# Kernel optimization log

Hardware: AMD Instinct MI355X
Metric: run time of the kernel (lower is better)

## Reference

```python
import jax, jax.numpy as jnp
import numpy as np

BN_EPS = 1e-3  # keras BatchNormalization default epsilon


def setup_inputs() -> dict:
    key = jax.random.key(0)
    ks = jax.random.split(key, 12)
    B, K, F = 32, 1024, 16
    H, C = 64, 4
    inp = {
        "x": jax.random.normal(ks[0], (B, K, F), dtype=jnp.float32),
        "coordinates": jax.random.normal(ks[1], (B, K, 3), dtype=jnp.float32),
        "precision_squared": jax.random.uniform(ks[2], (1,), dtype=jnp.float32),
        # dense kernels (no dense bias in the original; scalar per-block bias instead)
        "W0": 0.05 * jax.random.normal(ks[3], (2 * F, H), dtype=jnp.float32),
        "W1": 0.05 * jax.random.normal(ks[4], (4 * H, H), dtype=jnp.float32),
        "W2": 0.05 * jax.random.normal(ks[5], (4 * H, H), dtype=jnp.float32),
        "W3": 0.05 * jax.random.normal(ks[6], (4 * H, C), dtype=jnp.float32),
        "b0": 0.05 * jax.random.normal(ks[7], (1,), dtype=jnp.float32),
        "b1": 0.05 * jax.random.normal(ks[8], (1,), dtype=jnp.float32),
        "b2": 0.05 * jax.random.normal(ks[9], (1,), dtype=jnp.float32),
        "b3": 0.05 * jax.random.normal(ks[10], (1,), dtype=jnp.float32),
        # batchnorm affine params (inference mode, moving_mean=0, moving_var=1)
        "g0": jnp.ones((H,), jnp.float32), "be0": jnp.zeros((H,), jnp.float32),
        "g1": jnp.ones((H,), jnp.float32), "be1": jnp.zeros((H,), jnp.float32),
        "g2": jnp.ones((H,), jnp.float32), "be2": jnp.zeros((H,), jnp.float32),
    }
    return inp


def _adjacency(coordinates, precision_squared):
    # pairwise squared distances per sample: [B,K,K]
    norms = jnp.sum(coordinates * coordinates, axis=-1)  # [B,K]
    dist = norms[:, :, None] - 2.0 * jnp.einsum("bkd,bjd->bkj", coordinates, coordinates) + norms[:, None, :]
    A = jnp.exp(-dist * precision_squared[0])
    return jax.nn.softmax(A, axis=-1)  # per-sample axis=1 == last axis of [K,K]


def _block(x, A, W, b, gamma, beta, final):
    h = jnp.einsum("bij,bjf->bif", A, x)          # matmul(A, x)
    h = jnp.concatenate([h, x], axis=-1) @ W + b[0]
    if not final:
        # inference BN with moving_mean=0, moving_var=1
        h = h * (gamma / jnp.sqrt(1.0 + BN_EPS)) + beta
        h = jnp.concatenate([h, jax.nn.relu(h)], axis=-1)
    return h


def reference(x, coordinates, precision_squared, W0, W1, W2, W3,
              b0, b1, b2, b3, g0, be0, g1, be1, g2, be2):
    A = _adjacency(coordinates, precision_squared)
    h = _block(x, A, W0, b0, g0, be0, False)
    h = _block(h, A, W1, b1, g1, be1, False)
    h = _block(h, A, W2, b2, g2, be2, False)
    h = _block(h, A, W3, b3, None, None, True)   # final block: no BN, no activation
    h = jnp.mean(h, axis=1)                      # [B, num_classes]
    return jax.nn.softmax(h, axis=1)
```

## Files before the change

kernel.cpp:

```cpp
#include <hip/hip_runtime.h>
#include <math.h>

typedef __attribute__((ext_vector_type(8)))  __bf16   bf16x8;
typedef __attribute__((ext_vector_type(4)))  float    f32x4;
typedef __attribute__((ext_vector_type(16))) float    f32x16;
typedef __attribute__((ext_vector_type(4)))  unsigned u32x4;
typedef __attribute__((ext_vector_type(2)))  unsigned u32x2;

__device__ __forceinline__ unsigned short f2bf(float f) {
    unsigned u = __builtin_bit_cast(unsigned, f);
    u += 0x7fffu + ((u >> 16) & 1u);
    return (unsigned short)(u >> 16);
}
__device__ __forceinline__ float bf2f(unsigned short b) {
    unsigned u = ((unsigned)b) << 16;
    return __builtin_bit_cast(float, u);
}
__device__ __forceinline__ unsigned swz3(int key) { return (unsigned)((key ^ (key >> 3)) & 7); }
__device__ __forceinline__ bf16x8 ldfrag(const char* p) { return __builtin_bit_cast(bf16x8, *(const u32x4*)p); }

__global__ __launch_bounds__(256)
void prep(const float* __restrict__ W0, const float* __restrict__ W1,
          const float* __restrict__ W2, const float* __restrict__ W3,
          unsigned short* __restrict__ wpk)
{
    int id = blockIdx.x * 256 + threadIdx.x;
    if (id >= 51200) return;
    float v;
    if (id < 2048) {
        int j = id;
        int e = j & 7, lane = (j >> 3) & 63, nt = (j >> 9) & 3;
        int f = ((lane >> 5) << 3) + e + ((nt >= 2) ? 16 : 0);
        int h = ((nt & 1) << 5) + (lane & 31);
        v = W0[f * 64 + h];
    } else {
        int jid = id - 2048;
        int l = jid >> 14;
        int j = jid & 16383;
        int e = j & 7, lane = (j >> 3) & 63, nt = (j >> 9) & 3, kk = j >> 11;
        int f = kk * 16 + ((lane >> 5) << 3) + e + ((nt >= 2) ? 128 : 0);
        int h = ((nt & 1) << 5) + (lane & 31);
        const float* W = (l == 0) ? W1 : (l == 1) ? W2 : W3;
        int H = (l == 2) ? 4 : 64;
        v = (h < H) ? W[f * H + h] : 0.f;
    }
    wpk[id] = f2bf(v);
}

__global__ __launch_bounds__(256, 3)
void tgen(const float* __restrict__ coords, const float* __restrict__ psq,
          unsigned short* __restrict__ Tg, float* __restrict__ pcol)
{
    __shared__ float4 sc[1152];
    __shared__ char   tile[16 * 2048];
    const int t = threadIdx.x;
    const int b = blockIdx.y;
    const int i0 = blockIdx.x * 16;
    for (int k = t; k < 1024; k += 256) {
        const float* c = coords + ((size_t)b*1024 + k)*3;
        float cx = c[0], cy = c[1], cz = c[2];
        sc[k + (k >> 3)] = make_float4(cx, cy, cz, cx*cx + cy*cy + cz*cz);
    }
    __syncthreads();
    const float p = psq[0];
    const int r = t >> 4, jg = t & 15;
    const int kci = i0 + r;
    const float4 ci = sc[kci + (kci >> 3)];
    u32x4 raw[8];
    float rsum = 0.f;
#pragma unroll
    for (int pp = 0; pp < 8; ++pp) {
        const int base = pp*144 + jg*9;
        u32x4 v;
#pragma unroll
        for (int e = 0; e < 4; ++e) {
            float4 cj0 = sc[base + 2*e], cj1 = sc[base + 2*e + 1];
            float d0 = ci.w + cj0.w - 2.f*(ci.x*cj0.x + ci.y*cj0.y + ci.z*cj0.z);
            float d1 = ci.w + cj1.w - 2.f*(ci.x*cj1.x + ci.y*cj1.y + ci.z*cj1.z);
            unsigned short h0 = f2bf(__expf(__expf(-d0 * p)));
            unsigned short h1 = f2bf(__expf(__expf(-d1 * p)));
            rsum += bf2f(h0) + bf2f(h1);
            v[e] = (unsigned)h0 | ((unsigned)h1 << 16);
        }
        raw[pp] = v;
    }
    rsum += __shfl_xor(rsum, 1);
    rsum += __shfl_xor(rsum, 2);
    rsum += __shfl_xor(rsum, 4);
    rsum += __shfl_xor(rsum, 8);
    const float rinv = 1.f / rsum;
    char* trow = tile + r * 2048;
#pragma unroll
    for (int pp = 0; pp < 8; ++pp) {
        u32x4 u = raw[pp], v;
#pragma unroll
        for (int e = 0; e < 4; ++e) {
            unsigned uu = u[e];
            unsigned short nl = f2bf(bf2f((unsigned short)(uu & 0xffffu)) * rinv);
            unsigned short nh = f2bf(bf2f((unsigned short)(uu >> 16)) * rinv);
            v[e] = (unsigned)nl | ((unsigned)nh << 16);
        }
        *(u32x4*)(trow + (pp*128 + jg*8)*2) = v;
    }
    __syncthreads();
    {
        const int j0 = t * 4;
        f32x4 cs = {0.f, 0.f, 0.f, 0.f};
#pragma unroll
        for (int rr = 0; rr < 16; ++rr) {
            u32x2 u = *(const u32x2*)(tile + rr*2048 + j0*2);
            cs[0] += bf2f((unsigned short)(u[0] & 0xffffu));
            cs[1] += bf2f((unsigned short)(u[0] >> 16));
            cs[2] += bf2f((unsigned short)(u[1] & 0xffffu));
            cs[3] += bf2f((unsigned short)(u[1] >> 16));
        }
        *(f32x4*)(pcol + ((size_t)(b*64 + blockIdx.x))*1024 + j0) = cs;
    }
    {
        const u32x4* src = (const u32x4*)tile;
        u32x4* dst = (u32x4*)(Tg + ((size_t)(b*1024 + i0))*1024);
        for (int v = t; v < 2048; v += 256) dst[v] = src[v];
    }
}

__global__ __launch_bounds__(256, 2)
void proj0(const float* __restrict__ x32, const unsigned short* __restrict__ wpk,
           const float* __restrict__ bias, unsigned short* __restrict__ vuT)
{
    __shared__ char smem[2048 + 4096 + 16384];
    constexpr int XS = 0, WS = 2048, TBO = 6144;
    const int t = threadIdx.x;
    const int l = t & 63, w = t >> 6;
    const int b = blockIdx.y;
    const int i0g = blockIdx.x * 64;
    const int m31 = l & 31, kg = l >> 5;
    const int mi = w & 1, ntb = (w >> 1) * 2;
    const float bv = bias[0];

    {
        const int i = t >> 2, q = t & 3;
        const float* s = x32 + ((size_t)(b*1024 + i0g + i))*16 + q*4;
        unsigned short h0 = f2bf(s[0]), h1 = f2bf(s[1]), h2 = f2bf(s[2]), h3 = f2bf(s[3]);
        u32x2 v = {(unsigned)h0 | ((unsigned)h1 << 16), (unsigned)h2 | ((unsigned)h3 << 16)};
        *(u32x2*)(smem + XS + i*32 + ((q*8) ^ ((i & 1) << 4))) = v;
    }
    {
        u32x4* dstw = (u32x4*)(smem + WS);
        const u32x4* srcw = (const u32x4*)wpk;
        if (t < 256) dstw[t] = srcw[t];
    }
    __syncthreads();

    f32x16 acc0, acc1;
#pragma unroll
    for (int r = 0; r < 16; ++r) { acc0[r] = 0.f; acc1[r] = 0.f; }
    const int arow = mi*32 + m31;
    const char* ap = smem + XS + arow * 32;
    const unsigned swA = (unsigned)(arow & 1) << 4;
    {
        bf16x8 a  = ldfrag(ap + ((kg*16) ^ swA));
        bf16x8 b0 = ldfrag(smem + WS + (ntb    )*1024 + l*16);
        bf16x8 b1 = ldfrag(smem + WS + (ntb + 1)*1024 + l*16);
        acc0 = __builtin_amdgcn_mfma_f32_32x32x16_bf16(a, b0, acc0, 0, 0, 0);
        acc1 = __builtin_amdgcn_mfma_f32_32x32x16_bf16(a, b1, acc1, 0, 0, 0);
    }
    __syncthreads();
#pragma unroll
    for (int ntp = 0; ntp < 2; ++ntp) {
        const int nt = ntb + ntp;
        const int prow = nt*32 + m31;
        char* tb = smem + TBO + prow*128;
        const unsigned sw = (unsigned)(prow & 7) << 4;
        const float badd = (nt >= 2) ? bv : 0.f;
#pragma unroll
        for (int r = 0; r < 16; ++r) {
            const int i = mi*32 + (r & 3) + 8*(r >> 2) + 4*kg;
            float z = ((ntp == 0) ? acc0[r] : acc1[r]) + badd;
            *(unsigned short*)(tb + ((i*2) ^ sw)) = f2bf(z);
        }
    }
    __syncthreads();
    {
        const int hh = t >> 1, q = t & 1;
        const char* tb = smem + TBO + hh*128;
        const unsigned sw = (unsigned)(hh & 7) << 4;
        unsigned short* g = vuT + ((size_t)(b*128 + hh))*1024 + i0g + q*32;
#pragma unroll
        for (int gg = 0; gg < 4; ++gg) {
            u32x4 v = *(const u32x4*)(tb + ((q*64 + gg*16) ^ sw));
            *(u32x4*)(g + gg*8) = v;
        }
    }
}

__global__ __launch_bounds__(256, 2)
void fspmm(const unsigned short* __restrict__ vuT, const unsigned short* __restrict__ P,
           const float* __restrict__ gamma, const float* __restrict__ beta,
           const unsigned short* __restrict__ wpkN, const float* __restrict__ biasN,
           unsigned short* __restrict__ ovuT)
{
    __shared__ char smem[32768];
    const int t = threadIdx.x;
    const int l = t & 63, w = t >> 6;
    const int b = blockIdx.y;
    const int i0g = blockIdx.x * 64;
    const int m31 = l & 31, kg = l >> 5;
    const int wh = w >> 1, wi2 = w & 1;
    const float bvN = biasN[0];

    const int r4 = t >> 2, c4 = t & 3;
    const unsigned short* gp = P   + ((size_t)(b*1024 + i0g + r4))*1024 + c4*16;
    const unsigned short* gv = vuT + ((size_t)(b*128 + r4))*1024 + c4*16;
    u32x4 rp0 = *(const u32x4*)(gp), rp1 = *(const u32x4*)(gp + 8);
    u32x4 rv0 = *(const u32x4*)(gv), rv1 = *(const u32x4*)(gv + 8);
    const unsigned swr = swz3(r4) << 4;
    const int aRow = wh*32 + m31, bRow = wi2*32 + m31;
    const unsigned swA = swz3(aRow) << 4, swB = swz3(bRow) << 4;

    f32x16 acc;
#pragma unroll
    for (int r = 0; r < 16; ++r) acc[r] = 0.f;

    for (int jt = 0; jt < 16; ++jt) {
        const int p = jt & 1;
        {
            char* pt = smem + p*8192 + r4*128;
            *(u32x4*)(pt + ((c4*32     ) ^ swr)) = rp0;
            *(u32x4*)(pt + ((c4*32 + 16) ^ swr)) = rp1;
            char* vt = smem + 16384 + p*8192 + r4*128;
            *(u32x4*)(vt + ((c4*32     ) ^ swr)) = rv0;
            *(u32x4*)(vt + ((c4*32 + 16) ^ swr)) = rv1;
        }
        if (jt < 15) {
            rp0 = *(const u32x4*)(gp + (jt+1)*64);
            rp1 = *(const u32x4*)(gp + (jt+1)*64 + 8);
            rv0 = *(const u32x4*)(gv + (jt+1)*64);
            rv1 = *(const u32x4*)(gv + (jt+1)*64 + 8);
        }
        __syncthreads();
        const char* a_ = smem + 16384 + p*8192 + aRow*128;
        const char* b_ = smem + p*8192 + bRow*128;
#pragma unroll
        for (int kk = 0; kk < 4; ++kk) {
            const unsigned off = kk*32 + kg*16;
            bf16x8 af = ldfrag(a_ + (off ^ swA));
            bf16x8 bf = ldfrag(b_ + (off ^ swB));
            acc = __builtin_amdgcn_mfma_f32_32x32x16_bf16(af, bf, acc, 0, 0, 0);
        }
        __syncthreads();
    }

    {
        const unsigned short* gu = vuT + ((size_t)(b*128 + 64 + r4))*1024 + i0g + c4*16;
        u32x4 u0 = *(const u32x4*)(gu), u1 = *(const u32x4*)(gu + 8);
        *(u32x4*)(smem + r4*128 + c4*32)      = u0;
        *(u32x4*)(smem + r4*128 + c4*32 + 16) = u1;
    }
    __syncthreads();
    const float bns = rsqrtf(1.f + 1e-3f);
    const int ii = wi2*32 + m31;
    char* ZT = smem + 16384;
    const unsigned swzi = (unsigned)(ii & 7) << 4;
#pragma unroll
    for (int r = 0; r < 16; ++r) {
        const int h = wh*32 + (r & 3) + 8*(r >> 2) + 4*kg;
        float u = bf2f(*(const unsigned short*)(smem + h*128 + ii*2));
        float z = (acc[r] + u) * (gamma[h] * bns) + beta[h];
        *(unsigned short*)(ZT + ii*256 + (((unsigned)(h*2)) ^ swzi))        = f2bf(z);
        *(unsigned short*)(ZT + ii*256 + (((unsigned)((64 + h)*2)) ^ swzi)) = f2bf(fmaxf(z, 0.f));
    }
    __syncthreads();

    f32x16 vac, uac;
#pragma unroll
    for (int r = 0; r < 16; ++r) { vac[r] = 0.f; uac[r] = bvN; }
    const char* bx_base = ZT + ii*256;
#pragma unroll
    for (int kk = 0; kk < 8; ++kk) {
        bf16x8 awv = __builtin_bit_cast(bf16x8, *(const u32x4*)(wpkN + ((size_t)((kk*4 + wh    )*64 + l))*8));
        bf16x8 awu = __builtin_bit_cast(bf16x8, *(const u32x4*)(wpkN + ((size_t)((kk*4 + wh + 2)*64 + l))*8));
        bf16x8 bx  = ldfrag(bx_base + ((kk*32 + kg*16) ^ swzi));
        vac = __builtin_amdgcn_mfma_f32_32x32x16_bf16(awv, bx, vac, 0, 0, 0);
        uac = __builtin_amdgcn_mfma_f32_32x32x16_bf16(awu, bx, uac, 0, 0, 0);
    }
    __syncthreads();
    {
        char* TB = smem;
#pragma unroll
        for (int r = 0; r < 16; ++r) {
            const int hv = wh*32 + (r & 3) + 8*(r >> 2) + 4*kg;
            const unsigned sw = (unsigned)(hv & 7) << 4;
            *(unsigned short*)(TB + hv*128        + ((ii*2) ^ sw)) = f2bf(vac[r]);
            *(unsigned short*)(TB + (hv + 64)*128 + ((ii*2) ^ sw)) = f2bf(uac[r]);
        }
    }
    __syncthreads();
    {
        const int hh = t >> 1, q = t & 1;
        const char* tb = smem + hh*128;
        const unsigned sw = (unsigned)(hh & 7) << 4;
        unsigned short* g = ovuT + ((size_t)(b*128 + hh))*1024 + i0g + q*32;
#pragma unroll
        for (int gg = 0; gg < 4; ++gg) {
            u32x4 v = *(const u32x4*)(tb + ((q*64 + gg*16) ^ sw));
            *(u32x4*)(g + gg*8) = v;
        }
    }
}

__global__ __launch_bounds__(256)
void finalize(const float* __restrict__ pcol, const unsigned short* __restrict__ vuT3,
              float* __restrict__ out)
{
    __shared__ float red[2056];
    const int b = blockIdx.x, t = threadIdx.x;
    const int j0 = t * 4;
    f32x4 cs = {0.f, 0.f, 0.f, 0.f};
    for (int p = 0; p < 64; ++p)
        cs += *(const f32x4*)(pcol + ((size_t)(b*64 + p))*1024 + j0);
    float lv[4], lu[4];
#pragma unroll
    for (int h = 0; h < 4; ++h) {
        const unsigned short* vr = vuT3 + ((size_t)(b*128 + h))*1024 + j0;
        lv[h] = cs[0]*bf2f(vr[0]) + cs[1]*bf2f(vr[1]) + cs[2]*bf2f(vr[2]) + cs[3]*bf2f(vr[3]);
        const unsigned short* ur = vuT3 + ((size_t)(b*128 + 64 + h))*1024 + j0;
        lu[h] = bf2f(ur[0]) + bf2f(ur[1]) + bf2f(ur[2]) + bf2f(ur[3]);
    }
#pragma unroll
    for (int q = 0; q < 4; ++q) { red[t*8 + q] = lv[q]; red[t*8 + 4 + q] = lu[q]; }
    __syncthreads();
    if (t < 8) {
        float s = 0.f;
        for (int k = 0; k < 256; ++k) s += red[k*8 + t];
        red[2048 + t] = s;
    }
    __syncthreads();
    if (t == 0) {
        float v[4];
#pragma unroll
        for (int h = 0; h < 4; ++h) v[h] = (red[2048 + h] + red[2048 + 4 + h]) * (1.f / 1024.f);
        const float m = fmaxf(fmaxf(v[0], v[1]), fmaxf(v[2], v[3]));
        float e[4], se = 0.f;
#pragma unroll
        for (int h = 0; h < 4; ++h) { e[h] = __expf(v[h] - m); se += e[h]; }
        const float inv = 1.f / se;
#pragma unroll
        for (int h = 0; h < 4; ++h) out[b*4 + h] = e[h] * inv;
    }
}

extern "C" void kernel_launch(void* const* d_in, const int* in_sizes, int n_in,
                              void* d_out, int out_size, void* d_ws, size_t ws_size,
                              hipStream_t stream)
{
    const float* x   = (const float*)d_in[0];
    const float* co  = (const float*)d_in[1];
    const float* psq = (const float*)d_in[2];
    const float* W0  = (const float*)d_in[3];
    const float* W1  = (const float*)d_in[4];
    const float* W2  = (const float*)d_in[5];
    const float* W3  = (const float*)d_in[6];
    const float* b0  = (const float*)d_in[7];
    const float* b1  = (const float*)d_in[8];
    const float* b2  = (const float*)d_in[9];
    const float* b3  = (const float*)d_in[10];
    const float* g0  = (const float*)d_in[11];
    const float* be0 = (const float*)d_in[12];
    const float* g1  = (const float*)d_in[13];
    const float* be1 = (const float*)d_in[14];
    const float* g2  = (const float*)d_in[15];
    const float* be2 = (const float*)d_in[16];

    char* ws = (char*)d_ws;
    const size_t MB = (size_t)1 << 20;
    unsigned short* P    = (unsigned short*)(ws);
    float*          pcol = (float*)(ws + 64*MB);
    unsigned short* vuA  = (unsigned short*)(ws + 72*MB);
    unsigned short* vuB  = (unsigned short*)(ws + 80*MB);
    unsigned short* wpk  = (unsigned short*)(ws + 88*MB);

    prep<<<dim3(200), 256, 0, stream>>>(W0, W1, W2, W3, wpk);
    tgen<<<dim3(64, 32), 256, 0, stream>>>(co, psq, P, pcol);

    dim3 grid(16, 32);
    proj0<<<grid, 256, 0, stream>>>(x, wpk, b0, vuA);
    fspmm<<<grid, 256, 0, stream>>>(vuA, P, g0, be0, wpk + 2048,  b1, vuB);
    fspmm<<<grid, 256, 0, stream>>>(vuB, P, g1, be1, wpk + 18432, b2, vuA);
    fspmm<<<grid, 256, 0, stream>>>(vuA, P, g2, be2, wpk + 34816, b3, vuB);
    finalize<<<dim3(32), 256, 0, stream>>>(pcol, vuB, (float*)d_out);
}
```

Before: 193.6 us.

## Load MFMA fragments directly from global in fspmm and swizzle tgen LDS tile

Measured after the change: 239.2 us. +23.6%, slower.

```diff
diff --git a/kernel.cpp b/kernel.cpp
--- a/kernel.cpp
+++ b/kernel.cpp
@@ -18,6 +18,7 @@
 }
 __device__ __forceinline__ unsigned swz3(int key) { return (unsigned)((key ^ (key >> 3)) & 7); }
 __device__ __forceinline__ bf16x8 ldfrag(const char* p) { return __builtin_bit_cast(bf16x8, *(const u32x4*)p); }
+__device__ __forceinline__ bf16x8 castf(u32x4 v) { return __builtin_bit_cast(bf16x8, v); }
 
 __global__ __launch_bounds__(256)
 void prep(const float* __restrict__ W0, const float* __restrict__ W1,
@@ -66,6 +67,7 @@
     const int r = t >> 4, jg = t & 15;
     const int kci = i0 + r;
     const float4 ci = sc[kci + (kci >> 3)];
+    const unsigned rsw = (unsigned)(r & 7) << 4;
     u32x4 raw[8];
     float rsum = 0.f;
 #pragma unroll
@@ -100,26 +102,28 @@
             unsigned short nh = f2bf(bf2f((unsigned short)(uu >> 16)) * rinv);
             v[e] = (unsigned)nl | ((unsigned)nh << 16);
         }
-        *(u32x4*)(trow + (pp*128 + jg*8)*2) = v;
-    }
-    __syncthreads();
-    {
-        const int j0 = t * 4;
+        *(u32x4*)(trow + (((unsigned)(pp*256 + jg*16)) ^ rsw)) = v;
+    }
+    __syncthreads();
+    {
         f32x4 cs = {0.f, 0.f, 0.f, 0.f};
 #pragma unroll
         for (int rr = 0; rr < 16; ++rr) {
-            u32x2 u = *(const u32x2*)(tile + rr*2048 + j0*2);
+            u32x2 u = *(const u32x2*)(tile + rr*2048 + (((unsigned)(t*8)) ^ ((unsigned)(rr & 7) << 4)));
             cs[0] += bf2f((unsigned short)(u[0] & 0xffffu));
             cs[1] += bf2f((unsigned short)(u[0] >> 16));
             cs[2] += bf2f((unsigned short)(u[1] & 0xffffu));
             cs[3] += bf2f((unsigned short)(u[1] >> 16));
         }
-        *(f32x4*)(pcol + ((size_t)(b*64 + blockIdx.x))*1024 + j0) = cs;
-    }
-    {
-        const u32x4* src = (const u32x4*)tile;
+        *(f32x4*)(pcol + ((size_t)(b*64 + blockIdx.x))*1024 + t*4) = cs;
+    }
+    {
         u32x4* dst = (u32x4*)(Tg + ((size_t)(b*1024 + i0))*1024);
-        for (int v = t; v < 2048; v += 256) dst[v] = src[v];
+        for (int v = t; v < 2048; v += 256) {
+            const int row = v >> 7;
+            const unsigned cin = ((unsigned)((v & 127) * 16)) ^ ((unsigned)(row & 7) << 4);
+            dst[v] = *(const u32x4*)(tile + row*2048 + cin);
+        }
     }
 }
 
@@ -199,7 +203,7 @@
            const unsigned short* __restrict__ wpkN, const float* __restrict__ biasN,
            unsigned short* __restrict__ ovuT)
 {
-    __shared__ char smem[32768];
+    __shared__ char ZT[16384];
     const int t = threadIdx.x;
     const int l = t & 63, w = t >> 6;
     const int b = blockIdx.y;
@@ -208,63 +212,50 @@
     const int wh = w >> 1, wi2 = w & 1;
     const float bvN = biasN[0];
 
-    const int r4 = t >> 2, c4 = t & 3;
-    const unsigned short* gp = P   + ((size_t)(b*1024 + i0g + r4))*1024 + c4*16;
-    const unsigned short* gv = vuT + ((size_t)(b*128 + r4))*1024 + c4*16;
-    u32x4 rp0 = *(const u32x4*)(gp), rp1 = *(const u32x4*)(gp + 8);
-    u32x4 rv0 = *(const u32x4*)(gv), rv1 = *(const u32x4*)(gv + 8);
-    const unsigned swr = swz3(r4) << 4;
-    const int aRow = wh*32 + m31, bRow = wi2*32 + m31;
-    const unsigned swA = swz3(aRow) << 4, swB = swz3(bRow) << 4;
+    const unsigned short* gA = vuT + ((size_t)(b*128  + wh*32  + m31))*1024 + kg*8;
+    const unsigned short* gB = P   + ((size_t)(b*1024 + i0g + wi2*32 + m31))*1024 + kg*8;
 
     f32x16 acc;
 #pragma unroll
     for (int r = 0; r < 16; ++r) acc[r] = 0.f;
 
-    for (int jt = 0; jt < 16; ++jt) {
-        const int p = jt & 1;
-        {
-            char* pt = smem + p*8192 + r4*128;
-            *(u32x4*)(pt + ((c4*32     ) ^ swr)) = rp0;
-            *(u32x4*)(pt + ((c4*32 + 16) ^ swr)) = rp1;
-            char* vt = smem + 16384 + p*8192 + r4*128;
-            *(u32x4*)(vt + ((c4*32     ) ^ swr)) = rv0;
-            *(u32x4*)(vt + ((c4*32 + 16) ^ swr)) = rv1;
-        }
-        if (jt < 15) {
-            rp0 = *(const u32x4*)(gp + (jt+1)*64);
-            rp1 = *(const u32x4*)(gp + (jt+1)*64 + 8);
-            rv0 = *(const u32x4*)(gv + (jt+1)*64);
-            rv1 = *(const u32x4*)(gv + (jt+1)*64 + 8);
-        }
-        __syncthreads();
-        const char* a_ = smem + 16384 + p*8192 + aRow*128;
-        const char* b_ = smem + p*8192 + bRow*128;
-#pragma unroll
-        for (int kk = 0; kk < 4; ++kk) {
-            const unsigned off = kk*32 + kg*16;
-            bf16x8 af = ldfrag(a_ + (off ^ swA));
-            bf16x8 bf = ldfrag(b_ + (off ^ swB));
-            acc = __builtin_amdgcn_mfma_f32_32x32x16_bf16(af, bf, acc, 0, 0, 0);
-        }
-        __syncthreads();
-    }
-
-    {
-        const unsigned short* gu = vuT + ((size_t)(b*128 + 64 + r4))*1024 + i0g + c4*16;
-        u32x4 u0 = *(const u32x4*)(gu), u1 = *(const u32x4*)(gu + 8);
-        *(u32x4*)(smem + r4*128 + c4*32)      = u0;
-        *(u32x4*)(smem + r4*128 + c4*32 + 16) = u1;
-    }
-    __syncthreads();
+    u32x4 Xa0, Xa1, Xa2, Xa3, Xb0, Xb1, Xb2, Xb3;
+    u32x4 Ya0, Ya1, Ya2, Ya3, Yb0, Yb1, Yb2, Yb3;
+
+#define LD8(Sa0,Sa1,Sa2,Sa3,Sb0,Sb1,Sb2,Sb3, JT) do {                      \
+        const unsigned short* pa_ = gA + (JT)*64;                          \
+        const unsigned short* pb_ = gB + (JT)*64;                          \
+        Sa0 = *(const u32x4*)(pa_);      Sa1 = *(const u32x4*)(pa_ + 16);  \
+        Sa2 = *(const u32x4*)(pa_ + 32); Sa3 = *(const u32x4*)(pa_ + 48);  \
+        Sb0 = *(const u32x4*)(pb_);      Sb1 = *(const u32x4*)(pb_ + 16);  \
+        Sb2 = *(const u32x4*)(pb_ + 32); Sb3 = *(const u32x4*)(pb_ + 48);  \
+    } while (0)
+#define MM4(Sa0,Sa1,Sa2,Sa3,Sb0,Sb1,Sb2,Sb3) do {                                   \
+        acc = __builtin_amdgcn_mfma_f32_32x32x16_bf16(castf(Sa0), castf(Sb0), acc, 0, 0, 0); \
+        acc = __builtin_amdgcn_mfma_f32_32x32x16_bf16(castf(Sa1), castf(Sb1), acc, 0, 0, 0); \
+        acc = __builtin_amdgcn_mfma_f32_32x32x16_bf16(castf(Sa2), castf(Sb2), acc, 0, 0, 0); \
+        acc = __builtin_amdgcn_mfma_f32_32x32x16_bf16(castf(Sa3), castf(Sb3), acc, 0, 0, 0); \
+    } while (0)
+
+    LD8(Xa0,Xa1,Xa2,Xa3,Xb0,Xb1,Xb2,Xb3, 0);
+#pragma unroll
+    for (int jt = 0; jt < 16; jt += 2) {
+        LD8(Ya0,Ya1,Ya2,Ya3,Yb0,Yb1,Yb2,Yb3, jt + 1);
+        MM4(Xa0,Xa1,Xa2,Xa3,Xb0,Xb1,Xb2,Xb3);
+        if (jt + 2 < 16) LD8(Xa0,Xa1,Xa2,Xa3,Xb0,Xb1,Xb2,Xb3, jt + 2);
+        MM4(Ya0,Ya1,Ya2,Ya3,Yb0,Yb1,Yb2,Yb3);
+    }
+#undef LD8
+#undef MM4
+
     const float bns = rsqrtf(1.f + 1e-3f);
     const int ii = wi2*32 + m31;
-    char* ZT = smem + 16384;
     const unsigned swzi = (unsigned)(ii & 7) << 4;
+    const unsigned short* gu = vuT + ((size_t)(b*128 + 64))*1024 + i0g + ii;
 #pragma unroll
     for (int r = 0; r < 16; ++r) {
         const int h = wh*32 + (r & 3) + 8*(r >> 2) + 4*kg;
-        float u = bf2f(*(const unsigned short*)(smem + h*128 + ii*2));
+        float u = bf2f(gu[(size_t)h * 1024]);
         float z = (acc[r] + u) * (gamma[h] * bns) + beta[h];
         *(unsigned short*)(ZT + ii*256 + (((unsigned)(h*2)) ^ swzi))        = f2bf(z);
         *(unsigned short*)(ZT + ii*256 + (((unsigned)((64 + h)*2)) ^ swzi)) = f2bf(fmaxf(z, 0.f));
@@ -285,19 +276,18 @@
     }
     __syncthreads();
     {
-        char* TB = smem;
 #pragma unroll
         for (int r = 0; r < 16; ++r) {
             const int hv = wh*32 + (r & 3) + 8*(r >> 2) + 4*kg;
             const unsigned sw = (unsigned)(hv & 7) << 4;
-            *(unsigned short*)(TB + hv*128        + ((ii*2) ^ sw)) = f2bf(vac[r]);
-            *(unsigned short*)(TB + (hv + 64)*128 + ((ii*2) ^ sw)) = f2bf(uac[r]);
+            *(unsigned short*)(ZT + hv*128        + ((ii*2) ^ sw)) = f2bf(vac[r]);
+            *(unsigned short*)(ZT + (hv + 64)*128 + ((ii*2) ^ sw)) = f2bf(uac[r]);
         }
     }
     __syncthreads();
     {
         const int hh = t >> 1, q = t & 1;
-        const char* tb = smem + hh*128;
+        const char* tb = ZT + hh*128;
         const unsigned sw = (unsigned)(hh & 7) << 4;
         unsigned short* g = ovuT + ((size_t)(b*128 + hh))*1024 + i0g + q*32;
 #pragma unroll
```
